# Performance work log

Hardware: AMD Instinct MI355X
Metric: run time of the kernel (lower is better)

Reference implementation:

```python
import jax, jax.numpy as jnp
import numpy as np

# Layered type graph: L layers of M nodes; layer 0 = basic types, layers >=1 reference earlier layers only.
L, M, D, P, S = 64, 2048, 128, 4, 2
NB = 11  # number of Kotlin basic types (kotlin.Any ... kotlin.Unit)
N = L * M


def setup_inputs() -> dict:
    key = jax.random.key(0)
    ks = jax.random.split(key, 8)
    rng = np.random.default_rng(0)
    basic_names = jnp.asarray(rng.integers(0, NB, size=(M,)), dtype=jnp.int32)
    # properties / superTypes point strictly to earlier layers (valid topological DAG)
    prop_ids = np.zeros((L, M, P), dtype=np.int32)
    super_ids = np.zeros((L, M, S), dtype=np.int32)
    for l in range(1, L):
        prop_ids[l] = rng.integers(0, l * M, size=(M, P))
        super_ids[l] = rng.integers(0, l * M, size=(M, S))
    prop_ids = jnp.asarray(prop_ids)
    super_ids = jnp.asarray(super_ids)
    sc = 0.05
    return {
        "basic_names": basic_names,
        "prop_ids": prop_ids,
        "super_ids": super_ids,
        "basic_table": jax.random.normal(ks[0], (NB, D), jnp.float32) * sc,
        "W_m": jax.random.normal(ks[1], (D, 4 * D), jnp.float32) * sc,
        "U_m": jax.random.normal(ks[2], (D, 4 * D), jnp.float32) * sc,
        "b_m": jnp.zeros((4 * D,), jnp.float32),
        "W_s": jax.random.normal(ks[3], (D, 4 * D), jnp.float32) * sc,
        "U_s": jax.random.normal(ks[4], (D, 4 * D), jnp.float32) * sc,
        "b_s": jnp.zeros((4 * D,), jnp.float32),
        "empty_members": jax.random.normal(ks[5], (D,), jnp.float32) * sc,
    }


def _lstm_last(seq, W, U, b):
    # seq: [T, B, D]; keras LSTM (tanh / sigmoid, gate order i,f,g,o); returns last hidden [B, D]
    T, B, Dh = seq.shape
    h = jnp.zeros((B, Dh), seq.dtype)
    c = jnp.zeros((B, Dh), seq.dtype)
    for t in range(T):  # T is a small static constant (P+1 or S+1)
        z = seq[t] @ W + h @ U + b  # [B, 4D]
        i, f, g, o = jnp.split(z, 4, axis=-1)
        c = jax.nn.sigmoid(f) * c + jax.nn.sigmoid(i) * jnp.tanh(g)
        h = jax.nn.sigmoid(o) * jnp.tanh(c)
    return h


def reference(basic_names, prop_ids, super_ids, basic_table, W_m, U_m, b_m, W_s, U_s, b_s, empty_members):
    emb = jnp.zeros((N, D), basic_table.dtype)
    emb = emb.at[:M].set(basic_table[basic_names])  # layer 0: basic type embedding lookup

    def step(emb, xs):
        l, pid, sid = xs  # pid:[M,P] sid:[M,S], all indices < l*M (already computed)
        prop_e = jnp.swapaxes(emb[pid], 0, 1)  # [P, M, D] irregular gather
        seq_m = jnp.concatenate([jnp.broadcast_to(empty_members, (1, M, D)), prop_e], axis=0)  # [P+1, M, D]
        h_m = _lstm_last(seq_m, W_m, U_m, b_m)  # embed_members
        sup_e = jnp.swapaxes(emb[sid], 0, 1)  # [S, M, D]
        seq_s = jnp.concatenate([sup_e, h_m[None]], axis=0)  # [S+1, M, D]
        h_s = _lstm_last(seq_s, W_s, U_s, b_s)  # embed_super_types
        emb = jax.lax.dynamic_update_slice(emb, h_s, (l * M, 0))
        return emb, None

    ls = jnp.arange(1, L, dtype=jnp.int32)
    emb, _ = jax.lax.scan(step, emb, (ls, prop_ids[1:], super_ids[1:]))
    return emb  # [N, D] == tf.convert_to_tensor(class_embeddings)
```

## Files before the change

kernel.cpp:

```cpp
#include <hip/hip_runtime.h>

typedef unsigned short u16;
typedef short s16x8 __attribute__((ext_vector_type(8)));
typedef float f32x4 __attribute__((ext_vector_type(4)));

#define LAYERS   64
#define M_NODES  2048
#define DIM      128
#define FD       512
#define CHUNK    16
#define NBLK     128
#define TPB      512
#define XPAD     136

__device__ __forceinline__ u16 f2bf(float f) {
    union { float f; unsigned int i; } v; v.f = f;
    unsigned int r = (v.i + 0x7FFFu + ((v.i >> 16) & 1u)) >> 16;
    return (u16)r;
}
__device__ __forceinline__ float bf2f(u16 h) {
    union { unsigned int i; float f; } v; v.i = ((unsigned int)h) << 16;
    return v.f;
}
__device__ __forceinline__ float sigm(float x) {
    return __builtin_amdgcn_rcpf(1.0f + __builtin_exp2f(-1.44269504f * x));
}
__device__ __forceinline__ float tanh_f(float x) {
    float ax = __builtin_fabsf(x);
    float t  = __builtin_exp2f(-2.88539008f * ax);
    float r  = (1.0f - t) * __builtin_amdgcn_rcpf(1.0f + t);
    return __builtin_copysignf(r, x);
}

__global__ void l0_kernel(const int* __restrict__ names, const float* __restrict__ table,
                          float* __restrict__ emb) {
    int v = blockIdx.x * blockDim.x + threadIdx.x;
    if (v >= M_NODES * (DIM / 4)) return;
    int row = v >> 5, c = v & 31;
    const float4* src = (const float4*)(table + (size_t)names[row] * DIM);
    ((float4*)(emb + (size_t)row * DIM))[c] = src[c];
}

__global__ void repack_kernel(const float* __restrict__ Wm, const float* __restrict__ Um,
                              const float* __restrict__ Ws, const float* __restrict__ Us,
                              u16* __restrict__ packed) {
    int t = blockIdx.x * blockDim.x + threadIdx.x;
    if (t >= 4 * 4 * 32 * 64) return;
    int lane = t & 63, ntg = (t >> 6) & 31, kc = (t >> 11) & 3, mat = t >> 13;
    const float* B = (mat == 0) ? Wm : (mat == 1) ? Um : (mat == 2) ? Ws : Us;
    int q = lane >> 4, nl = lane & 15;
    int kb = kc * 32 + q * 8;
    int n  = ntg * 16 + nl;
    u16* dst = packed + ((((size_t)mat * 4 + kc) * 32 + ntg) * 64 + lane) * 8;
    #pragma unroll
    for (int j = 0; j < 8; j++) dst[j] = f2bf(B[(size_t)(kb + j) * FD + n]);
}

__global__ void init_t0_kernel(const float* __restrict__ Wm, const float* __restrict__ Um,
                               const float* __restrict__ bm, const float* __restrict__ empty,
                               float* __restrict__ t0buf) {
    __shared__ float h1s[DIM];
    int dd = threadIdx.x;
    if (dd < DIM) {
        float z0 = bm[dd], z1 = bm[256 + dd], z2 = bm[384 + dd];
        for (int k = 0; k < DIM; k++) {
            float e = empty[k];
            const float* Wr = Wm + (size_t)k * FD;
            z0 += e * Wr[dd];
            z1 += e * Wr[256 + dd];
            z2 += e * Wr[384 + dd];
        }
        float c1 = sigm(z0) * tanh_f(z1);
        float h1 = sigm(z2) * tanh_f(c1);
        t0buf[dd] = c1;
        h1s[dd] = h1;
    }
    __syncthreads();
    if (dd < DIM) {
        float u0 = 0.f, u1 = 0.f, u2 = 0.f, u3 = 0.f;
        for (int k = 0; k < DIM; k++) {
            float hb = bf2f(f2bf(h1s[k]));
            const float* Ur = Um + (size_t)k * FD;
            u0 += hb * bf2f(f2bf(Ur[dd]));
            u1 += hb * bf2f(f2bf(Ur[128 + dd]));
            u2 += hb * bf2f(f2bf(Ur[256 + dd]));
            u3 += hb * bf2f(f2bf(Ur[384 + dd]));
        }
        t0buf[128 + 0 * 128 + dd] = u0;
        t0buf[128 + 1 * 128 + dd] = u1;
        t0buf[128 + 2 * 128 + dd] = u2;
        t0buf[128 + 3 * 128 + dd] = u3;
    }
}

__global__ __launch_bounds__(TPB, 1) void layer5_kernel(
    float* __restrict__ emb, const int* __restrict__ prop_ids, const int* __restrict__ super_ids,
    const float* __restrict__ bm, const float* __restrict__ bs,
    const u16* __restrict__ packed, const float* __restrict__ t0buf, int l) {

    __shared__ __align__(16) u16 xs[6][CHUNK][XPAD];
    __shared__ __align__(16) u16 hbM[2][CHUNK][XPAD];
    __shared__ __align__(16) u16 hbS[2][CHUNK][XPAD];

    const int tid  = threadIdx.x;
    const int b    = blockIdx.x;
    const int g0   = b * CHUNK;
    const int wv   = tid >> 6;
    const int lane = tid & 63;
    const int q    = lane >> 4, nl = lane & 15;
    const int d    = wv * 16 + nl;

    auto ldB = [&](int mat, int kc, int g) -> s16x8 {
        return *(const s16x8*)(packed + ((((size_t)mat * 4 + kc) * 32 + (g * 8 + wv)) * 64 + lane) * 8);
    };
    auto load_afrag = [&](const u16* X , int kc) -> s16x8 {
        return *(const s16x8*)(X + (size_t)nl * XPAD + kc * 32 + q * 8);
    };

    if (tid < 384) {
        int quarter = tid & 3;
        int r    = tid >> 2;
        int slot = r >> 4;
        int node = r & 15;
        size_t idx;
        if (slot < 4) idx = (size_t)prop_ids [((size_t)l * M_NODES + g0 + node) * 4 + slot];
        else          idx = (size_t)super_ids[((size_t)l * M_NODES + g0 + node) * 2 + (slot - 4)];
        const f32x4* src = (const f32x4*)(emb + idx * DIM) + quarter * 8;
        u16* dst = &xs[slot][node][0];
        int e0 = quarter * 32;
        #pragma unroll
        for (int j = 0; j < 8; j++) {
            f32x4 v = src[j];
            ushort4 w;
            w.x = f2bf(v[0]); w.y = f2bf(v[1]); w.z = f2bf(v[2]); w.w = f2bf(v[3]);
            *(ushort4*)(dst + e0 + j * 4) = w;
        }
    }

    float bzm[4], bzs[4], uh1[4];
    #pragma unroll
    for (int g = 0; g < 4; g++) {
        bzm[g] = bm[g * 128 + d];
        bzs[g] = bs[g * 128 + d];
        uh1[g] = t0buf[128 + g * 128 + d];
    }
    const float c1 = t0buf[d];

    s16x8 wfs[4][4];
    #pragma unroll
    for (int kc = 0; kc < 4; kc++)
        #pragma unroll
        for (int g = 0; g < 4; g++) wfs[kc][g] = ldB(2, kc, g);

    __syncthreads();

    auto gates = [&](const f32x4* acc, const float* bz, float* cc, int mode, int parity) {
        #pragma unroll
        for (int r2 = 0; r2 < 4; r2++) {
            int m = q * 4 + r2;
            float zi = acc[0][r2] + bz[0];
            float zf = acc[1][r2] + bz[1];
            float zg = acc[2][r2] + bz[2];
            float zo = acc[3][r2] + bz[3];
            float c  = sigm(zf) * cc[r2] + sigm(zi) * tanh_f(zg);
            cc[r2] = c;
            float h  = sigm(zo) * tanh_f(c);
            if (mode == 0)      hbM[parity][m][d] = f2bf(h);
            else if (mode == 3) hbS[parity][m][d] = f2bf(h);
            else if (mode == 1) xs[0][m][d] = f2bf(h);
            else emb[((size_t)l * M_NODES + g0 + m) * DIM + d] = h;
        }
    };

    f32x4 zxs0[4], zxs1[4];
    #pragma unroll
    for (int g = 0; g < 4; g++) { zxs0[g] = (f32x4){0.f,0.f,0.f,0.f}; zxs1[g] = (f32x4){0.f,0.f,0.f,0.f}; }
    #pragma unroll
    for (int kc = 0; kc < 4; kc++) {
        s16x8 a4 = load_afrag(&xs[4][0][0], kc);
        s16x8 a5 = load_afrag(&xs[5][0][0], kc);
        #pragma unroll
        for (int g = 0; g < 4; g++) {
            zxs0[g] = __builtin_amdgcn_mfma_f32_16x16x32_bf16(a4, wfs[kc][g], zxs0[g], 0, 0, 0);
            zxs1[g] = __builtin_amdgcn_mfma_f32_16x16x32_bf16(a5, wfs[kc][g], zxs1[g], 0, 0, 0);
        }
    }
    f32x4 zxm[4][4];
    {
        s16x8 wfm[4][4];
        #pragma unroll
        for (int kc = 0; kc < 4; kc++)
            #pragma unroll
            for (int g = 0; g < 4; g++) wfm[kc][g] = ldB(0, kc, g);
        #pragma unroll
        for (int s = 0; s < 4; s++) {
            #pragma unroll
            for (int g = 0; g < 4; g++) zxm[s][g] = (f32x4){0.f, 0.f, 0.f, 0.f};
            #pragma unroll
            for (int kc = 0; kc < 4; kc++) {
                s16x8 a = load_afrag(&xs[s][0][0], kc);
                #pragma unroll
                for (int g = 0; g < 4; g++)
                    zxm[s][g] = __builtin_amdgcn_mfma_f32_16x16x32_bf16(a, wfm[kc][g], zxm[s][g], 0, 0, 0);
            }
        }
    }

    s16x8 ufm[4][4];
    #pragma unroll
    for (int kc = 0; kc < 4; kc++)
        #pragma unroll
        for (int g = 0; g < 4; g++) ufm[kc][g] = ldB(1, kc, g);

    float ccm[4] = {c1, c1, c1, c1};
    float ccs[4] = {0.f, 0.f, 0.f, 0.f};

    {
        f32x4 accM[4];
        #pragma unroll
        for (int g = 0; g < 4; g++) accM[g] = zxm[0][g] + uh1[g];
        gates(accM, bzm, ccm, 0, 1);
        gates(zxs0, bzs, ccs, 3, 0);
    }
    __syncthreads();

    {
        f32x4 acc[4];
        #pragma unroll
        for (int g = 0; g < 4; g++) acc[g] = zxm[1][g];
        #pragma unroll
        for (int kc = 0; kc < 4; kc++) {
            s16x8 a = load_afrag(&hbM[1][0][0], kc);
            #pragma unroll
            for (int g = 0; g < 4; g++)
                acc[g] = __builtin_amdgcn_mfma_f32_16x16x32_bf16(a, ufm[kc][g], acc[g], 0, 0, 0);
        }
        gates(acc, bzm, ccm, 0, 0);
    }
    __syncthreads();

    s16x8 ufs[4][4];
    #pragma unroll
    for (int kc = 0; kc < 4; kc++)
        #pragma unroll
        for (int g = 0; g < 4; g++) ufs[kc][g] = ldB(3, kc, g);

    {
        f32x4 am[4], as_[4];
        #pragma unroll
        for (int g = 0; g < 4; g++) { am[g] = zxm[2][g]; as_[g] = zxs1[g]; }
        #pragma unroll
        for (int kc = 0; kc < 4; kc++) {
            s16x8 aM = load_afrag(&hbM[0][0][0], kc);
            s16x8 aS = load_afrag(&hbS[0][0][0], kc);
            #pragma unroll
            for (int g = 0; g < 4; g++) {
                am[g]  = __builtin_amdgcn_mfma_f32_16x16x32_bf16(aM, ufm[kc][g], am[g],  0, 0, 0);
                as_[g] = __builtin_amdgcn_mfma_f32_16x16x32_bf16(aS, ufs[kc][g], as_[g], 0, 0, 0);
            }
        }
        gates(am,  bzm, ccm, 0, 1);
        gates(as_, bzs, ccs, 3, 1);
    }
    __syncthreads();

    {
        f32x4 acc[4];
        #pragma unroll
        for (int g = 0; g < 4; g++) acc[g] = zxm[3][g];
        #pragma unroll
        for (int kc = 0; kc < 4; kc++) {
            s16x8 a = load_afrag(&hbM[1][0][0], kc);
            #pragma unroll
            for (int g = 0; g < 4; g++)
                acc[g] = __builtin_amdgcn_mfma_f32_16x16x32_bf16(a, ufm[kc][g], acc[g], 0, 0, 0);
        }
        gates(acc, bzm, ccm, 1, 0);
    }
    __syncthreads();

    {
        s16x8 wfs2[4][4];
        #pragma unroll
        for (int kc = 0; kc < 4; kc++)
            #pragma unroll
            for (int g = 0; g < 4; g++) wfs2[kc][g] = ldB(2, kc, g);
        f32x4 acc[4];
        #pragma unroll
        for (int g = 0; g < 4; g++) acc[g] = (f32x4){0.f, 0.f, 0.f, 0.f};
        #pragma unroll
        for (int kc = 0; kc < 4; kc++) {
            s16x8 a0 = load_afrag(&xs[0][0][0], kc);
            s16x8 aS = load_afrag(&hbS[1][0][0], kc);
            #pragma unroll
            for (int g = 0; g < 4; g++) {
                acc[g] = __builtin_amdgcn_mfma_f32_16x16x32_bf16(a0, wfs2[kc][g], acc[g], 0, 0, 0);
                acc[g] = __builtin_amdgcn_mfma_f32_16x16x32_bf16(aS, ufs[kc][g],  acc[g], 0, 0, 0);
            }
        }
        gates(acc, bzs, ccs, 2, 0);
    }
}

__global__ __launch_bounds__(TPB, 1) void layer_kernel_direct(
    float* __restrict__ emb, const int* __restrict__ prop_ids, const int* __restrict__ super_ids,
    const float* __restrict__ Wm, const float* __restrict__ Um, const float* __restrict__ bm,
    const float* __restrict__ Ws, const float* __restrict__ Us, const float* __restrict__ bs,
    const float* __restrict__ empty, int l) {

    __shared__ __align__(16) u16  xs[6][CHUNK][XPAD];
    __shared__ __align__(16) u16  hbuf[2][CHUNK][XPAD];
    __shared__ __align__(16) u16  empty_s[XPAD];

    const int tid  = threadIdx.x;
    const int b    = blockIdx.x;
    const int g0   = b * CHUNK;
    const size_t row0 = (size_t)l * M_NODES + g0;

    const int wv   = tid >> 6;
    const int lane = tid & 63;
    const int q    = lane >> 4, nl = lane & 15;
    const int d    = wv * 16 + nl;

    if (tid < 384) {
        int quarter = tid & 3;
        int r    = tid >> 2;
        int slot = r >> 4;
        int node = r & 15;
        size_t idx;
        if (slot < 4) idx = (size_t)prop_ids [((size_t)l * M_NODES + g0 + node) * 4 + slot];
        else          idx = (size_t)super_ids[((size_t)l * M_NODES + g0 + node) * 2 + (slot - 4)];
        const float4* src = (const float4*)(emb + idx * DIM);
        u16* dst = &xs[slot][node][0];
        int e0 = quarter * 32;
        #pragma unroll
        for (int j = 0; j < 8; j++) {
            float4 v = src[(e0 >> 2) + j];
            int o = e0 + j * 4;
            dst[o] = f2bf(v.x); dst[o + 1] = f2bf(v.y);
            dst[o + 2] = f2bf(v.z); dst[o + 3] = f2bf(v.w);
        }
    } else if (tid < 384 + 128) {
        int dd = tid - 384;
        empty_s[dd] = f2bf(empty[dd]);
    }
    __syncthreads();

    auto load_bfrag_direct = [&](const float* B, int kc, int g) -> s16x8 {
        int kb = kc * 32 + q * 8;
        int n  = g * 128 + d;
        s16x8 f;
        #pragma unroll
        for (int j = 0; j < 8; j++) f[j] = (short)f2bf(B[(size_t)(kb + j) * FD + n]);
        return f;
    };
    auto load_afrag = [&](const u16* X, int kc) -> s16x8 {
        return *(const s16x8*)(X + (size_t)nl * XPAD + kc * 32 + q * 8);
    };

    auto run_phase = [&](const float* Wg, const float* Ug, const float* bias,
                         int nsteps, const int* slots, bool write_hm, bool write_out) {
        s16x8 wf[4][4], uf[4][4];
        #pragma unroll
        for (int kc = 0; kc < 4; kc++) {
            #pragma unroll
            for (int g = 0; g < 4; g++) {
                wf[kc][g] = load_bfrag_direct(Wg, kc, g);
                uf[kc][g] = load_bfrag_direct(Ug, kc, g);
            }
        }
        float bz[4];
        #pragma unroll
        for (int g = 0; g < 4; g++) bz[g] = bias[g * 128 + d];
        float cc[4] = {0.f, 0.f, 0.f, 0.f};

        #pragma unroll 1
        for (int t = 0; t < nsteps; t++) {
            int s = slots[t];
            f32x4 acc[4];
            #pragma unroll
            for (int g = 0; g < 4; g++) acc[g] = (f32x4){0.f, 0.f, 0.f, 0.f};
            #pragma unroll
            for (int kc = 0; kc < 4; kc++) {
                s16x8 a = (s < 0) ? *(const s16x8*)(&empty_s[kc * 32 + q * 8])
                                  : load_afrag(&xs[s][0][0], kc);
                #pragma unroll
                for (int g = 0; g < 4; g++)
                    acc[g] = __builtin_amdgcn_mfma_f32_16x16x32_bf16(a, wf[kc][g], acc[g], 0, 0, 0);
            }
            if (t > 0) {
                __syncthreads();
                const u16* hb = &hbuf[(t - 1) & 1][0][0];
                #pragma unroll
                for (int kc = 0; kc < 4; kc++) {
                    s16x8 a = load_afrag(hb, kc);
                    #pragma unroll
                    for (int g = 0; g < 4; g++)
                        acc[g] = __builtin_amdgcn_mfma_f32_16x16x32_bf16(a, uf[kc][g], acc[g], 0, 0, 0);
                }
            }
            bool last = (t == nsteps - 1);
            #pragma unroll
            for (int r2 = 0; r2 < 4; r2++) {
                int m = q * 4 + r2;
                float zi = acc[0][r2] + bz[0];
                float zf = acc[1][r2] + bz[1];
                float zg = acc[2][r2] + bz[2];
                float zo = acc[3][r2] + bz[3];
                float c  = sigm(zf) * cc[r2] + sigm(zi) * tanh_f(zg);
                cc[r2] = c;
                float h  = sigm(zo) * tanh_f(c);
                if (!last)          hbuf[t & 1][m][d] = f2bf(h);
                else if (write_hm)  xs[0][m][d] = f2bf(h);
                else if (write_out) emb[(row0 + m) * DIM + d] = h;
            }
        }
    };

    {
        const int slots_m[5] = {-1, 0, 1, 2, 3};
        run_phase(Wm, Um, bm, 5, slots_m, true, false);
    }
    {
        const int slots_s[3] = {4, 5, 0};
        run_phase(Ws, Us, bs, 3, slots_s, false, true);
    }
}

extern "C" void kernel_launch(void* const* d_in, const int* in_sizes, int n_in,
                              void* d_out, int out_size, void* d_ws, size_t ws_size,
                              hipStream_t stream) {
    const int*   names = (const int*)d_in[0];
    const int*   pids  = (const int*)d_in[1];
    const int*   sids  = (const int*)d_in[2];
    const float* table = (const float*)d_in[3];
    const float* Wm    = (const float*)d_in[4];
    const float* Um    = (const float*)d_in[5];
    const float* bm    = (const float*)d_in[6];
    const float* Ws    = (const float*)d_in[7];
    const float* Us    = (const float*)d_in[8];
    const float* bs    = (const float*)d_in[9];
    const float* bsv   = bs;
    const float* empt  = (const float*)d_in[10];
    float* emb  = (float*)d_out;
    u16* packed = (u16*)d_ws;

    l0_kernel<<<256, 256, 0, stream>>>(names, table, emb);

    const size_t packed_bytes = (size_t)4 * 4 * 32 * 64 * 8 * sizeof(u16);
    const size_t t0_bytes     = 640 * sizeof(float);
    const bool ws_ok = ws_size >= packed_bytes + t0_bytes;

    if (ws_ok) {
        float* t0buf = (float*)((char*)d_ws + packed_bytes);
        repack_kernel<<<128, 256, 0, stream>>>(Wm, Um, Ws, Us, packed);
        init_t0_kernel<<<1, 128, 0, stream>>>(Wm, Um, bm, empt, t0buf);
        for (int l = 1; l < LAYERS; l++)
            layer5_kernel<<<NBLK, TPB, 0, stream>>>(emb, pids, sids, bm, bsv,
                                                    packed, t0buf, l);
    } else {
        for (int l = 1; l < LAYERS; l++)
            layer_kernel_direct<<<NBLK, TPB, 0, stream>>>(emb, pids, sids, Wm, Um, bm,
                                                          Ws, Us, bs, empt, l);
    }
}
```

Measured before the change: 1.089 ms.

## Keep a bf16 mirror of embeddings for gathers and merge setup kernels

Adds a bf16 copy of the embedding table in workspace, written alongside the fp32 output. Each layer gathers neighbour rows from this mirror instead of reading fp32 and converting, which halves gather bytes and drops the conversion work. The three setup kernels are also merged into one launch. The cost is extra bf16 stores on every layer and a dependence on a large workspace; if the workspace is too small, it falls back to the fp32 path.

Measured after the change: 1.050 ms. -3.5%, faster.

```diff
diff --git a/kernel.cpp b/kernel.cpp
--- a/kernel.cpp
+++ b/kernel.cpp
@@ -41,62 +41,80 @@
     ((float4*)(emb + (size_t)row * DIM))[c] = src[c];
 }
 
-__global__ void repack_kernel(const float* __restrict__ Wm, const float* __restrict__ Um,
-                              const float* __restrict__ Ws, const float* __restrict__ Us,
-                              u16* __restrict__ packed) {
-    int t = blockIdx.x * blockDim.x + threadIdx.x;
-    if (t >= 4 * 4 * 32 * 64) return;
-    int lane = t & 63, ntg = (t >> 6) & 31, kc = (t >> 11) & 3, mat = t >> 13;
-    const float* B = (mat == 0) ? Wm : (mat == 1) ? Um : (mat == 2) ? Ws : Us;
-    int q = lane >> 4, nl = lane & 15;
-    int kb = kc * 32 + q * 8;
-    int n  = ntg * 16 + nl;
-    u16* dst = packed + ((((size_t)mat * 4 + kc) * 32 + ntg) * 64 + lane) * 8;
-    #pragma unroll
-    for (int j = 0; j < 8; j++) dst[j] = f2bf(B[(size_t)(kb + j) * FD + n]);
-}
-
-__global__ void init_t0_kernel(const float* __restrict__ Wm, const float* __restrict__ Um,
-                               const float* __restrict__ bm, const float* __restrict__ empty,
-                               float* __restrict__ t0buf) {
-    __shared__ float h1s[DIM];
-    int dd = threadIdx.x;
-    if (dd < DIM) {
-        float z0 = bm[dd], z1 = bm[256 + dd], z2 = bm[384 + dd];
-        for (int k = 0; k < DIM; k++) {
-            float e = empty[k];
-            const float* Wr = Wm + (size_t)k * FD;
-            z0 += e * Wr[dd];
-            z1 += e * Wr[256 + dd];
-            z2 += e * Wr[384 + dd];
-        }
-        float c1 = sigm(z0) * tanh_f(z1);
-        float h1 = sigm(z2) * tanh_f(c1);
-        t0buf[dd] = c1;
-        h1s[dd] = h1;
-    }
-    __syncthreads();
-    if (dd < DIM) {
-        float u0 = 0.f, u1 = 0.f, u2 = 0.f, u3 = 0.f;
-        for (int k = 0; k < DIM; k++) {
-            float hb = bf2f(f2bf(h1s[k]));
-            const float* Ur = Um + (size_t)k * FD;
-            u0 += hb * bf2f(f2bf(Ur[dd]));
-            u1 += hb * bf2f(f2bf(Ur[128 + dd]));
-            u2 += hb * bf2f(f2bf(Ur[256 + dd]));
-            u3 += hb * bf2f(f2bf(Ur[384 + dd]));
-        }
-        t0buf[128 + 0 * 128 + dd] = u0;
-        t0buf[128 + 1 * 128 + dd] = u1;
-        t0buf[128 + 2 * 128 + dd] = u2;
-        t0buf[128 + 3 * 128 + dd] = u3;
-    }
-}
-
+template <bool MIRROR>
+__global__ void setup_kernel(const int* __restrict__ names, const float* __restrict__ table,
+                             float* __restrict__ emb,
+                             const float* __restrict__ Wm, const float* __restrict__ Um,
+                             const float* __restrict__ Ws, const float* __restrict__ Us,
+                             const float* __restrict__ bm, const float* __restrict__ empty,
+                             u16* __restrict__ packed, float* __restrict__ t0buf,
+                             u16* __restrict__ emb16) {
+    const int blk = blockIdx.x;
+    const int tid = threadIdx.x;
+    if (blk < 128) {
+        int t = blk * 256 + tid;
+        int lane = t & 63, ntg = (t >> 6) & 31, kc = (t >> 11) & 3, mat = t >> 13;
+        const float* B = (mat == 0) ? Wm : (mat == 1) ? Um : (mat == 2) ? Ws : Us;
+        int q = lane >> 4, nl = lane & 15;
+        int kb = kc * 32 + q * 8;
+        int n  = ntg * 16 + nl;
+        u16* dst = packed + ((((size_t)mat * 4 + kc) * 32 + ntg) * 64 + lane) * 8;
+        #pragma unroll
+        for (int j = 0; j < 8; j++) dst[j] = f2bf(B[(size_t)(kb + j) * FD + n]);
+    } else if (blk == 128) {
+        __shared__ float h1s[DIM];
+        int dd = tid;
+        if (dd < DIM) {
+            float z0 = bm[dd], z1 = bm[256 + dd], z2 = bm[384 + dd];
+            for (int k = 0; k < DIM; k++) {
+                float e = empty[k];
+                const float* Wr = Wm + (size_t)k * FD;
+                z0 += e * Wr[dd];
+                z1 += e * Wr[256 + dd];
+                z2 += e * Wr[384 + dd];
+            }
+            float c1 = sigm(z0) * tanh_f(z1);
+            float h1 = sigm(z2) * tanh_f(c1);
+            t0buf[dd] = c1;
+            h1s[dd] = h1;
+        }
+        __syncthreads();
+        if (dd < DIM) {
+            float u0 = 0.f, u1 = 0.f, u2 = 0.f, u3 = 0.f;
+            for (int k = 0; k < DIM; k++) {
+                float hb = bf2f(f2bf(h1s[k]));
+                const float* Ur = Um + (size_t)k * FD;
+                u0 += hb * bf2f(f2bf(Ur[dd]));
+                u1 += hb * bf2f(f2bf(Ur[128 + dd]));
+                u2 += hb * bf2f(f2bf(Ur[256 + dd]));
+                u3 += hb * bf2f(f2bf(Ur[384 + dd]));
+            }
+            t0buf[128 + 0 * 128 + dd] = u0;
+            t0buf[128 + 1 * 128 + dd] = u1;
+            t0buf[128 + 2 * 128 + dd] = u2;
+            t0buf[128 + 3 * 128 + dd] = u3;
+        }
+    } else {
+        int v = (blk - 129) * 256 + tid;
+        if (v >= M_NODES * (DIM / 4)) return;
+        int row = v >> 5, c = v & 31;
+        const float4* src = (const float4*)(table + (size_t)names[row] * DIM);
+        float4 vv = src[c];
+        ((float4*)(emb + (size_t)row * DIM))[c] = vv;
+        if (MIRROR) {
+            ushort4 w;
+            w.x = f2bf(vv.x); w.y = f2bf(vv.y); w.z = f2bf(vv.z); w.w = f2bf(vv.w);
+            *(ushort4*)(emb16 + (size_t)row * DIM + c * 4) = w;
+        }
+    }
+}
+
+template <bool MIRROR>
 __global__ __launch_bounds__(TPB, 1) void layer5_kernel(
     float* __restrict__ emb, const int* __restrict__ prop_ids, const int* __restrict__ super_ids,
     const float* __restrict__ bm, const float* __restrict__ bs,
-    const u16* __restrict__ packed, const float* __restrict__ t0buf, int l) {
+    const u16* __restrict__ packed, const float* __restrict__ t0buf,
+    u16* __restrict__ emb16, int l) {
 
     __shared__ __align__(16) u16 xs[6][CHUNK][XPAD];
     __shared__ __align__(16) u16 hbM[2][CHUNK][XPAD];
@@ -125,15 +143,22 @@
         size_t idx;
         if (slot < 4) idx = (size_t)prop_ids [((size_t)l * M_NODES + g0 + node) * 4 + slot];
         else          idx = (size_t)super_ids[((size_t)l * M_NODES + g0 + node) * 2 + (slot - 4)];
-        const f32x4* src = (const f32x4*)(emb + idx * DIM) + quarter * 8;
-        u16* dst = &xs[slot][node][0];
-        int e0 = quarter * 32;
-        #pragma unroll
-        for (int j = 0; j < 8; j++) {
-            f32x4 v = src[j];
-            ushort4 w;
-            w.x = f2bf(v[0]); w.y = f2bf(v[1]); w.z = f2bf(v[2]); w.w = f2bf(v[3]);
-            *(ushort4*)(dst + e0 + j * 4) = w;
+        if (MIRROR) {
+            const s16x8* src = (const s16x8*)(emb16 + idx * DIM) + quarter * 4;
+            u16* dst = &xs[slot][node][quarter * 32];
+            #pragma unroll
+            for (int j = 0; j < 4; j++) *(s16x8*)(dst + j * 8) = src[j];
+        } else {
+            const f32x4* src = (const f32x4*)(emb + idx * DIM) + quarter * 8;
+            u16* dst = &xs[slot][node][0];
+            int e0 = quarter * 32;
+            #pragma unroll
+            for (int j = 0; j < 8; j++) {
+                f32x4 v = src[j];
+                ushort4 w;
+                w.x = f2bf(v[0]); w.y = f2bf(v[1]); w.z = f2bf(v[2]); w.w = f2bf(v[3]);
+                *(ushort4*)(dst + e0 + j * 4) = w;
+            }
         }
     }
 
@@ -168,7 +193,10 @@
             if (mode == 0)      hbM[parity][m][d] = f2bf(h);
             else if (mode == 3) hbS[parity][m][d] = f2bf(h);
             else if (mode == 1) xs[0][m][d] = f2bf(h);
-            else emb[((size_t)l * M_NODES + g0 + m) * DIM + d] = h;
+            else {
+                emb[((size_t)l * M_NODES + g0 + m) * DIM + d] = h;
+                if (MIRROR) emb16[((size_t)l * M_NODES + g0 + m) * DIM + d] = f2bf(h);
+            }
         }
     };
 
@@ -440,25 +468,35 @@
     const float* Ws    = (const float*)d_in[7];
     const float* Us    = (const float*)d_in[8];
     const float* bs    = (const float*)d_in[9];
-    const float* bsv   = bs;
     const float* empt  = (const float*)d_in[10];
     float* emb  = (float*)d_out;
     u16* packed = (u16*)d_ws;
 
-    l0_kernel<<<256, 256, 0, stream>>>(names, table, emb);
-
     const size_t packed_bytes = (size_t)4 * 4 * 32 * 64 * 8 * sizeof(u16);
     const size_t t0_bytes     = 640 * sizeof(float);
-    const bool ws_ok = ws_size >= packed_bytes + t0_bytes;
-
-    if (ws_ok) {
+    const size_t mirror_off   = (size_t)1 << 20;
+    const size_t mirror_bytes = (size_t)LAYERS * M_NODES * DIM * sizeof(u16);
+    const bool ws_packed = ws_size >= packed_bytes + t0_bytes;
+    const bool ws_mirror = ws_size >= mirror_off + mirror_bytes;
+
+    if (ws_packed) {
         float* t0buf = (float*)((char*)d_ws + packed_bytes);
-        repack_kernel<<<128, 256, 0, stream>>>(Wm, Um, Ws, Us, packed);
-        init_t0_kernel<<<1, 128, 0, stream>>>(Wm, Um, bm, empt, t0buf);
-        for (int l = 1; l < LAYERS; l++)
-            layer5_kernel<<<NBLK, TPB, 0, stream>>>(emb, pids, sids, bm, bsv,
-                                                    packed, t0buf, l);
+        u16*   emb16 = ws_mirror ? (u16*)((char*)d_ws + mirror_off) : (u16*)nullptr;
+        if (ws_mirror) {
+            setup_kernel<true><<<385, 256, 0, stream>>>(names, table, emb, Wm, Um, Ws, Us,
+                                                        bm, empt, packed, t0buf, emb16);
+            for (int l = 1; l < LAYERS; l++)
+                layer5_kernel<true><<<NBLK, TPB, 0, stream>>>(emb, pids, sids, bm, bs,
+                                                              packed, t0buf, emb16, l);
+        } else {
+            setup_kernel<false><<<385, 256, 0, stream>>>(names, table, emb, Wm, Um, Ws, Us,
+                                                         bm, empt, packed, t0buf, emb16);
+            for (int l = 1; l < LAYERS; l++)
+                layer5_kernel<false><<<NBLK, TPB, 0, stream>>>(emb, pids, sids, bm, bs,
+                                                               packed, t0buf, emb16, l);
+        }
     } else {
+        l0_kernel<<<256, 256, 0, stream>>>(names, table, emb);
         for (int l = 1; l < LAYERS; l++)
             layer_kernel_direct<<<NBLK, TPB, 0, stream>>>(emb, pids, sids, Wm, Um, bm,
                                                           Ws, Us, bs, empt, l);
```
